# Kernel optimization log

Hardware: AMD Instinct MI355X
Metric: run time of the kernel (lower is better)

## Reference

```python
import jax, jax.numpy as jnp
import numpy as np

NUM_HEADS = 16

def setup_inputs() -> dict:
    key = jax.random.key(0)
    ks = jax.random.split(key, 6)
    S, B, D = 2048, 4, 1280
    return {
        "hidden_states": jax.random.normal(ks[0], (S, B, D), dtype=jnp.float32),
        "rotary_pos_emb": jax.random.normal(ks[1], (S, D // NUM_HEADS // 2), dtype=jnp.float32),
        "in_proj_w": jax.random.normal(ks[2], (3 * D, D), dtype=jnp.float32) * 0.02,
        "in_proj_b": jax.random.normal(ks[3], (3 * D,), dtype=jnp.float32) * 0.02,
        "out_proj_w": jax.random.normal(ks[4], (D, D), dtype=jnp.float32) * 0.02,
        "out_proj_b": jax.random.normal(ks[5], (D,), dtype=jnp.float32) * 0.02,
    }

def _rotate_half(x):
    h = x.shape[-1] // 2
    return jnp.concatenate([-x[..., h:], x[..., :h]], axis=-1)

def _apply_rope(t, cos, sin):
    # t: [B,S,H,Dh]; cos/sin: [1,S,1,Dh]. Compute in fp32 like the original.
    orig = t.dtype
    t32 = t.astype(jnp.float32)
    return (t32 * cos + _rotate_half(t32) * sin).astype(orig)

def reference(hidden_states, rotary_pos_emb, in_proj_w, in_proj_b, out_proj_w, out_proj_b):
    S, B, D = hidden_states.shape
    H = NUM_HEADS
    Dh = D // H

    # Fused QKV projection: [S,B,3D]
    qkv = jnp.einsum('sbd,ed->sbe', hidden_states, in_proj_w) + in_proj_b
    qkv = qkv.reshape(S, B, 3, H, Dh).transpose(2, 1, 0, 3, 4)  # [3,B,S,H,Dh]
    q, k, v = qkv[0], qkv[1], qkv[2]

    # RoPE tables: freqs [S, Dh/2] -> tiled to [1,S,1,Dh] (repeat along last dim)
    cos = jnp.tile(jnp.cos(rotary_pos_emb), (1, 2))[None, :, None, :].astype(jnp.float32)
    sin = jnp.tile(jnp.sin(rotary_pos_emb), (1, 2))[None, :, None, :].astype(jnp.float32)
    q = _apply_rope(q, cos, sin)
    k = _apply_rope(k, cos, sin)

    # [B,H,S,Dh]
    q = q.transpose(0, 2, 1, 3)
    k = k.transpose(0, 2, 1, 3)
    v = v.transpose(0, 2, 1, 3)

    scale = 1.0 / np.sqrt(Dh).astype(np.float32)
    scores = jnp.einsum('bhqd,bhkd->bhqk', q, k) * scale
    attn = jax.nn.softmax(scores, axis=-1)
    out = jnp.einsum('bhqk,bhkd->bhqd', attn, v)  # [B,H,S,Dh]

    out = out.transpose(2, 0, 1, 3).reshape(S, B, D)  # [S,B,D]
    return jnp.einsum('sbd,ed->sbe', out, out_proj_w) + out_proj_b
```

## Files before the change

kernel.cpp:

```cpp
#include <hip/hip_runtime.h>
#include <hip/hip_bf16.h>
#include <math.h>

typedef __bf16 bf16x4 __attribute__((ext_vector_type(4)));
typedef __bf16 bf16x8 __attribute__((ext_vector_type(8)));
typedef float  f32x4  __attribute__((ext_vector_type(4)));

#define S_LEN 2048
#define BATCH 4
#define DMODEL 1280
#define NHEAD 16
#define DHEAD 80
#define KDIM 1280

__device__ __forceinline__ f32x4 mfma_bf16(bf16x8 a, bf16x8 b, f32x4 c) {
  return __builtin_amdgcn_mfma_f32_16x16x32_bf16(a, b, c, 0, 0, 0);
}

__device__ __forceinline__ void gload16(const void* g, void* l) {
  __builtin_amdgcn_global_load_lds(
      (const __attribute__((address_space(1))) unsigned int*)g,
      (__attribute__((address_space(3))) unsigned int*)l, 16, 0, 0);
}

__global__ void cast_f32_to_bf16(const float* __restrict__ in,
                                 __bf16* __restrict__ out, int n4) {
  int i = blockIdx.x * 256 + threadIdx.x;
  if (i >= n4) return;
  float4 v = reinterpret_cast<const float4*>(in)[i];
  bf16x4 o;
  o[0] = (__bf16)v.x; o[1] = (__bf16)v.y; o[2] = (__bf16)v.z; o[3] = (__bf16)v.w;
  reinterpret_cast<bf16x4*>(out)[i] = o;
}

__global__ void build_sincos(const float* __restrict__ rot,
                             float* __restrict__ ctab, float* __restrict__ stab, int n) {
  int i = blockIdx.x * 256 + threadIdx.x;
  if (i >= n) return;
  float v = rot[i];
  ctab[i] = cosf(v);
  stab[i] = sinf(v);
}

__global__ void zero_fill(float* __restrict__ p, int n) {
  int i = blockIdx.x * 256 + threadIdx.x;
  if (i < n) p[i] = 0.0f;
}

__global__ __launch_bounds__(256, 4) void gemm_qkv128(
    const __bf16* __restrict__ A, const __bf16* __restrict__ Bw,
    const float* __restrict__ bias,
    __bf16* __restrict__ qw, __bf16* __restrict__ kw, __bf16* __restrict__ vtw)
{
  __shared__ __align__(1024) char smem[32768];
  const int tid = threadIdx.x;
  const int lane = tid & 63;
  const int w = tid >> 6;
  const int lr = lane & 15, lg = lane >> 4;
  const int wr = w >> 1, wc = w & 1;

  const int wg = blockIdx.x;
  const int xcd = wg & 7, idx = wg >> 3;
  const int bx = xcd * 8 + (idx & 7);
  const int by = idx >> 3;
  const int r0 = bx * 128, c0 = by * 128;
  const char* asrc = (const char*)(A + (size_t)r0 * KDIM);
  const char* bsrc = (const char*)(Bw + (size_t)c0 * KDIM);

  f32x4 acc[4][4] = {};

  for (int t = 0; t < 20; ++t) {
    const size_t kb = (size_t)t * 128;
#pragma unroll
    for (int i = 0; i < 8; ++i) {
      const int L = i * 4096 + tid * 16;
      const int r = (L & 16383) >> 7;
      const int coff = (L & 127) ^ ((r & 7) << 4);
      const char* s = (L < 16384 ? asrc : bsrc) + (size_t)r * 2560 + kb + coff;
      gload16(s, &smem[L]);
    }
    __syncthreads();

#pragma unroll
    for (int kk = 0; kk < 2; ++kk) {
      bf16x8 af[4], bfr[4];
#pragma unroll
      for (int rf = 0; rf < 4; ++rf) {
        const int row = wr * 64 + rf * 16 + lr;
        af[rf] = *reinterpret_cast<const bf16x8*>(
            &smem[row * 128 + ((kk * 64 + lg * 16) ^ ((row & 7) << 4))]);
      }
#pragma unroll
      for (int cf = 0; cf < 4; ++cf) {
        const int row = wc * 64 + cf * 16 + lr;
        bfr[cf] = *reinterpret_cast<const bf16x8*>(
            &smem[16384 + row * 128 + ((kk * 64 + lg * 16) ^ ((row & 7) << 4))]);
      }
#pragma unroll
      for (int rf = 0; rf < 4; ++rf)
#pragma unroll
        for (int cf = 0; cf < 4; ++cf)
          acc[rf][cf] = mfma_bf16(af[rf], bfr[cf], acc[rf][cf]);
    }
    __syncthreads();
  }

  float biasr[4];
#pragma unroll
  for (int cf = 0; cf < 4; ++cf) biasr[cf] = bias[c0 + wc * 64 + cf * 16 + lr];

#pragma unroll
  for (int cf = 0; cf < 4; ++cf) {
    const int col = wc * 64 + cf * 16 + lr;
#pragma unroll
    for (int rf = 0; rf < 4; ++rf)
#pragma unroll
      for (int j = 0; j < 4; ++j) {
        const int row = wr * 64 + rf * 16 + lg * 4 + j;
        *reinterpret_cast<__bf16*>(
            &smem[row * 256 + ((col ^ ((row & 7) << 3)) << 1)]) =
            (__bf16)(acc[rf][cf][j] + biasr[cf]);
      }
  }
  __syncthreads();

  const int which = c0 / DMODEL;
  const int ee0 = c0 - which * DMODEL;

  if (which < 2) {
    __bf16* dst = (which == 0) ? qw : kw;
#pragma unroll
    for (int i = 0; i < 8; ++i) {
      const int cid = i * 256 + tid;
      const int row = cid >> 4, slot = cid & 15;
      bf16x8 v = *reinterpret_cast<const bf16x8*>(
          &smem[row * 256 + ((slot ^ (row & 7)) << 4)]);
      const int tr = r0 + row;
      const int b = tr & 3, stok = tr >> 2;
      const int ee = ee0 + slot * 8;
      const int h = ee / DHEAD, dh = ee - h * DHEAD;
      *reinterpret_cast<bf16x8*>(
          &dst[((size_t)(b * NHEAD + h) * S_LEN + stok) * DHEAD + dh]) = v;
    }
  } else {
    const int s0 = r0 >> 2;
#pragma unroll
    for (int i = 0; i < 8; ++i) {
      const int cid = i * 256 + tid;
      const int col = cid >> 4;
      const int b = (cid >> 2) & 3, spblk = cid & 3;
      bf16x8 v;
#pragma unroll
      for (int k = 0; k < 8; ++k) {
        const int spl = spblk * 8 + k;
        const int sl = (spl & 3) | ((spl & 24) >> 1) | ((spl & 4) << 2);
        const int row = sl * 4 + b;
        v[k] = *reinterpret_cast<const __bf16*>(
            &smem[row * 256 + ((col ^ ((row & 7) << 3)) << 1)]);
      }
      const int ee = ee0 + col;
      const int h = ee / DHEAD, dh = ee - h * DHEAD;
      *reinterpret_cast<bf16x8*>(
          &vtw[((size_t)(b * NHEAD + h) * DHEAD + dh) * S_LEN + s0 + spblk * 8]) = v;
    }
  }
}

template <int MODE>
__global__ __launch_bounds__(256) void gemm_bt(
    const __bf16* __restrict__ A, const __bf16* __restrict__ Bw,
    const float* __restrict__ bias, float* __restrict__ outf)
{
  __shared__ __align__(16) char smem[2][2][16384];
  const int tid = threadIdx.x;
  const int lane = tid & 63;
  const int w = tid >> 6;
  const int lr = lane & 15, lg = lane >> 4;
  const int rowblk = (w >> 1) * 64, colblk = (w & 1) * 64;
  const int sxz = (lane & 7) << 4;

  const int wg = blockIdx.x;
  const int xcd = wg & 7, idx = wg >> 3;
  const int bx = xcd * 8 + (idx & 7);
  const int by = idx >> 3;
  const int r0 = bx * 128;
  const int c0 = by * 128;
  const char* asrc = (const char*)(A + (size_t)r0 * KDIM);
  const char* bsrc = (const char*)(Bw + (size_t)c0 * KDIM);

  f32x4 acc[4][4] = {};

  auto stage = [&](int buf, int kt) {
    const size_t kb = (size_t)kt * 128;
#pragma unroll
    for (int i = 0; i < 4; ++i) {
      int L = i * 4096 + tid * 16;
      int r = L >> 7;
      int coff = (L & 127) ^ ((r & 7) << 4);
      gload16(asrc + (size_t)r * 2560 + kb + coff, &smem[buf][0][L]);
      gload16(bsrc + (size_t)r * 2560 + kb + coff, &smem[buf][1][L]);
    }
  };

  auto compute = [&](int buf) {
#pragma unroll
    for (int kk = 0; kk < 2; ++kk) {
      const int cb = (kk * 64 + lg * 16) ^ sxz;
      bf16x8 af[4], bfr[4];
#pragma unroll
      for (int rf = 0; rf < 4; ++rf)
        af[rf] = *reinterpret_cast<const bf16x8*>(&smem[buf][0][(rowblk + rf * 16 + lr) * 128 + cb]);
#pragma unroll
      for (int cf = 0; cf < 4; ++cf)
        bfr[cf] = *reinterpret_cast<const bf16x8*>(&smem[buf][1][(colblk + cf * 16 + lr) * 128 + cb]);
#pragma unroll
      for (int rf = 0; rf < 4; ++rf)
#pragma unroll
        for (int cf = 0; cf < 4; ++cf)
          acc[rf][cf] = mfma_bf16(af[rf], bfr[cf], acc[rf][cf]);
    }
  };

  stage(0, 0);
  asm volatile("s_waitcnt vmcnt(0)" ::: "memory");
  __builtin_amdgcn_s_barrier();
  __builtin_amdgcn_sched_barrier(0);

  for (int t = 0; t < 20; ++t) {
    const int buf = t & 1;
    if (t < 19) {
      stage(buf ^ 1, t + 1);
      asm volatile("s_waitcnt vmcnt(8)" ::: "memory");
    } else {
      asm volatile("s_waitcnt vmcnt(0)" ::: "memory");
    }
    __builtin_amdgcn_sched_barrier(0);
    __builtin_amdgcn_s_barrier();
    __builtin_amdgcn_sched_barrier(0);

    compute(buf);

    __builtin_amdgcn_sched_barrier(0);
    __builtin_amdgcn_s_barrier();
    __builtin_amdgcn_sched_barrier(0);
  }

  float biasr[4];
#pragma unroll
  for (int cf = 0; cf < 4; ++cf) biasr[cf] = bias[c0 + colblk + cf * 16 + lr];

#pragma unroll
  for (int rf = 0; rf < 4; ++rf)
#pragma unroll
    for (int cf = 0; cf < 4; ++cf) {
      const int c = c0 + colblk + cf * 16 + lr;
#pragma unroll
      for (int j = 0; j < 4; ++j) {
        const int r = r0 + rowblk + rf * 16 + lg * 4 + j;
        outf[(size_t)r * DMODEL + c] = acc[rf][cf][j] + biasr[cf];
      }
    }
}

__global__ void rope_kernel(__bf16* __restrict__ qw, __bf16* __restrict__ kw,
                            const float* __restrict__ ctab, const float* __restrict__ stab,
                            float qscale)
{
  int idx = blockIdx.x * 256 + threadIdx.x;
  const int j = idx % 10;
  int rest = idx / 10;
  const int s = rest & (S_LEN - 1);
  rest >>= 11;
  const int bh = rest & 63;
  const int isk = rest >> 6;
  __bf16* base = (isk ? kw : qw) + ((size_t)bh * S_LEN + s) * DHEAD;
  const float4 c4 = *reinterpret_cast<const float4*>(ctab + s * 40 + j * 4);
  const float4 s4 = *reinterpret_cast<const float4*>(stab + s * 40 + j * 4);
  bf16x4 a = *reinterpret_cast<bf16x4*>(base + j * 4);
  bf16x4 b = *reinterpret_cast<bf16x4*>(base + 40 + j * 4);
  const float m = isk ? 1.0f : qscale;
  const float cc[4] = {c4.x, c4.y, c4.z, c4.w};
  const float ss[4] = {s4.x, s4.y, s4.z, s4.w};
#pragma unroll
  for (int t = 0; t < 4; ++t) {
    float fa = (float)a[t], fb = (float)b[t];
    a[t] = (__bf16)((fa * cc[t] - fb * ss[t]) * m);
    b[t] = (__bf16)((fb * cc[t] + fa * ss[t]) * m);
  }
  *reinterpret_cast<bf16x4*>(base + j * 4) = a;
  *reinterpret_cast<bf16x4*>(base + 40 + j * 4) = b;
}

__global__ __launch_bounds__(256, 2) void attn_kernel(
    const __bf16* __restrict__ qw, const __bf16* __restrict__ kw,
    const __bf16* __restrict__ vtw, __bf16* __restrict__ ow,
    const float* __restrict__ zp)
{
  __shared__ __align__(1024) char smem[2][24576];

  const int tid = threadIdx.x;
  const int lane = tid & 63;
  const int w = tid >> 6;
  const int lr = lane & 15, lg = lane >> 4;

  const int wg = blockIdx.x;
  const int local = wg >> 3;
  const int bh = (wg & 7) * 8 + (local >> 3);
  const int qt = local & 7;

  const char* qbase = (const char*)(qw + ((size_t)bh * S_LEN + qt * 256) * DHEAD);
  const char* kbase = (const char*)(kw + (size_t)bh * S_LEN * DHEAD);
  const char* vbase = (const char*)(vtw + (size_t)bh * DHEAD * S_LEN);
  const char* zpb = (const char*)zp;

  bf16x8 z8, one8;
#pragma unroll
  for (int i = 0; i < 8; ++i) { z8[i] = (__bf16)0.0f; one8[i] = (__bf16)1.0f; }

  bf16x8 aq[4][3];
#pragma unroll
  for (int m = 0; m < 4; ++m) {
    const char* rp = qbase + (size_t)(w * 64 + m * 16 + lr) * 160;
    aq[m][0] = *reinterpret_cast<const bf16x8*>(rp + lg * 16);
    aq[m][1] = *reinterpret_cast<const bf16x8*>(rp + 64 + lg * 16);
    aq[m][2] = (lg < 2) ? *reinterpret_cast<const bf16x8*>(rp + 128 + lg * 16) : z8;
  }

  const char* src[6];
  size_t step[6];
#pragma unroll
  for (int i = 0; i < 6; ++i) {
    const int s = w * 6 + i;
    if (s < 12) {
      const int ks = s >> 2, n = s & 3;
      if (ks == 2 && lg >= 2) { src[i] = zpb + lane * 16; step[i] = 0; }
      else { src[i] = kbase + (size_t)(n * 16 + lr) * 160 + ks * 64 + lg * 16; step[i] = 64 * 160; }
    } else {
      const int v = s - 12, mf = v >> 1, ks2 = v & 1;
      if (mf == 5) { src[i] = zpb + lane * 16; step[i] = 0; }
      else { src[i] = vbase + (size_t)(mf * 16 + lr) * 4096 + (size_t)(ks2 * 32 + lg * 8) * 2; step[i] = 128; }
    }
  }

  auto stage = [&](int buf) {
#pragma unroll
    for (int i = 0; i < 6; ++i) {
      gload16(src[i], &smem[buf][(w * 6 + i) * 1024]);
      src[i] += step[i];
    }
  };

  f32x4 accO[5][4] = {};
  f32x4 accD[4] = {};

  stage(0);
  asm volatile("s_waitcnt vmcnt(0)" ::: "memory");
  __builtin_amdgcn_s_barrier();
  __builtin_amdgcn_sched_barrier(0);

  for (int t = 0; t < 32; ++t) {
    const int buf = t & 1;
    if (t < 31) {
      stage(buf ^ 1);
      asm volatile("s_waitcnt vmcnt(6)" ::: "memory");
    } else {
      asm volatile("s_waitcnt vmcnt(0)" ::: "memory");
    }
    __builtin_amdgcn_sched_barrier(0);
    __builtin_amdgcn_s_barrier();
    __builtin_amdgcn_sched_barrier(0);

    const char* Kb = smem[buf];
    const char* Vb = smem[buf] + 12288;

    f32x4 sc[4][4] = {};
#pragma unroll
    for (int n = 0; n < 4; ++n) {
      bf16x8 af0 = *reinterpret_cast<const bf16x8*>(Kb + (0 * 4 + n) * 1024 + lane * 16);
      bf16x8 af1 = *reinterpret_cast<const bf16x8*>(Kb + (1 * 4 + n) * 1024 + lane * 16);
      bf16x8 af2 = *reinterpret_cast<const bf16x8*>(Kb + (2 * 4 + n) * 1024 + lane * 16);
#pragma unroll
      for (int m = 0; m < 4; ++m) {
        sc[m][n] = mfma_bf16(af0, aq[m][0], sc[m][n]);
        sc[m][n] = mfma_bf16(af1, aq[m][1], sc[m][n]);
        sc[m][n] = mfma_bf16(af2, aq[m][2], sc[m][n]);
      }
    }

    bf16x8 bp[4][2];
#pragma unroll
    for (int m = 0; m < 4; ++m)
#pragma unroll
      for (int n = 0; n < 4; ++n) {
#pragma unroll
        for (int j = 0; j < 4; ++j)
          bp[m][n >> 1][(n & 1) * 4 + j] = (__bf16)__builtin_amdgcn_exp2f(sc[m][n][j]);
      }

#pragma unroll
    for (int ks2 = 0; ks2 < 2; ++ks2) {
#pragma unroll
      for (int mf = 0; mf < 5; ++mf) {
        bf16x8 av = *reinterpret_cast<const bf16x8*>(Vb + (mf * 2 + ks2) * 1024 + lane * 16);
#pragma unroll
        for (int m = 0; m < 4; ++m)
          accO[mf][m] = mfma_bf16(av, bp[m][ks2], accO[mf][m]);
      }
#pragma unroll
      for (int m = 0; m < 4; ++m)
        accD[m] = mfma_bf16(one8, bp[m][ks2], accD[m]);
    }

    __builtin_amdgcn_sched_barrier(0);
    __builtin_amdgcn_s_barrier();
    __builtin_amdgcn_sched_barrier(0);
  }

  __syncthreads();

  float rinv[4];
#pragma unroll
  for (int m = 0; m < 4; ++m) rinv[m] = 1.0f / accD[m][0];

  char* sOut = smem[0];
#pragma unroll
  for (int mf = 0; mf < 5; ++mf)
#pragma unroll
    for (int m = 0; m < 4; ++m) {
      bf16x4 o4;
#pragma unroll
      for (int j = 0; j < 4; ++j) o4[j] = (__bf16)(accO[mf][m][j] * rinv[m]);
      *reinterpret_cast<bf16x4*>(sOut + (size_t)(w * 64 + m * 16 + lr) * 160 + (mf * 16 + lg * 4) * 2) = o4;
    }
  __syncthreads();

  const int b = bh >> 4, h = bh & 15;
#pragma unroll
  for (int i = 0; i < 10; ++i) {
    int c = i * 256 + tid;
    int row = c / 10, slot = c - row * 10;
    int token = (qt * 256 + row) * 4 + b;
    *reinterpret_cast<bf16x8*>((char*)ow + (size_t)token * 2560 + h * 160 + slot * 16) =
        *reinterpret_cast<const bf16x8*>(sOut + row * 160 + slot * 16);
  }
}

extern "C" void kernel_launch(void* const* d_in, const int* in_sizes, int n_in,
                              void* d_out, int out_size, void* d_ws, size_t ws_size,
                              hipStream_t stream)
{
  const float* hidden = (const float*)d_in[0];
  const float* rot    = (const float*)d_in[1];
  const float* w1     = (const float*)d_in[2];
  const float* b1     = (const float*)d_in[3];
  const float* w2     = (const float*)d_in[4];
  const float* b2     = (const float*)d_in[5];
  float* out = (float*)d_out;

  char* ws = (char*)d_ws;
  __bf16* Xbf  = (__bf16*)(ws);
  __bf16* W1bf = (__bf16*)(ws + 20971520);
  __bf16* W2bf = (__bf16*)(ws + 30801920);
  float*  ctab = (float*)(ws + 34078720);
  float*  stab = (float*)(ws + 34406400);
  __bf16* qwp  = (__bf16*)(ws + 34734080);
  __bf16* kwp  = (__bf16*)(ws + 55705600);
  __bf16* vtwp = (__bf16*)(ws + 76677120);
  __bf16* owp  = (__bf16*)(ws + 97648640);
  float*  zp   = (float*)(ws + 118620160);

  cast_f32_to_bf16<<<10240, 256, 0, stream>>>(hidden, Xbf, 2621440);
  cast_f32_to_bf16<<<4800, 256, 0, stream>>>(w1, W1bf, 1228800);
  cast_f32_to_bf16<<<1600, 256, 0, stream>>>(w2, W2bf, 409600);
  build_sincos<<<320, 256, 0, stream>>>(rot, ctab, stab, 81920);
  zero_fill<<<4, 256, 0, stream>>>(zp, 1024);

  gemm_qkv128<<<1920, 256, 0, stream>>>(Xbf, W1bf, b1, qwp, kwp, vtwp);

  const float qscale = 1.4426950408889634f / sqrtf(80.0f);
  rope_kernel<<<10240, 256, 0, stream>>>(qwp, kwp, ctab, stab, qscale);

  attn_kernel<<<512, 256, 0, stream>>>(qwp, kwp, vtwp, owp, zp);

  gemm_bt<1><<<640, 256, 0, stream>>>(owp, W2bf, b2, out);
}
```

Baseline: 247.6 us.

## Single-buffer output GEMM for higher occupancy and add MFMA priority hints in attention

The output projection GEMM drops double buffering in favour of a single 32KB LDS tile with plain __syncthreads, and sets launch_bounds to 4 blocks per CU. The aim is to hide memory latency through more resident workgroups rather than software prefetch. The attention kernel separately wraps its two MFMA phases in s_setprio so waves issuing matrix work get priority over waves doing exp2. The GEMM change gives up in-block load/compute overlap, and the priority hints may or may not change scheduling.

```diff
diff --git a/kernel.cpp b/kernel.cpp
--- a/kernel.cpp
+++ b/kernel.cpp
@@ -166,97 +166,75 @@
   }
 }
 
-template <int MODE>
-__global__ __launch_bounds__(256) void gemm_bt(
+__global__ __launch_bounds__(256, 4) void gemm_out128(
     const __bf16* __restrict__ A, const __bf16* __restrict__ Bw,
     const float* __restrict__ bias, float* __restrict__ outf)
 {
-  __shared__ __align__(16) char smem[2][2][16384];
+  __shared__ __align__(1024) char smem[32768];
   const int tid = threadIdx.x;
   const int lane = tid & 63;
   const int w = tid >> 6;
   const int lr = lane & 15, lg = lane >> 4;
-  const int rowblk = (w >> 1) * 64, colblk = (w & 1) * 64;
-  const int sxz = (lane & 7) << 4;
+  const int wr = w >> 1, wc = w & 1;
 
   const int wg = blockIdx.x;
   const int xcd = wg & 7, idx = wg >> 3;
   const int bx = xcd * 8 + (idx & 7);
   const int by = idx >> 3;
-  const int r0 = bx * 128;
-  const int c0 = by * 128;
+  const int r0 = bx * 128, c0 = by * 128;
   const char* asrc = (const char*)(A + (size_t)r0 * KDIM);
   const char* bsrc = (const char*)(Bw + (size_t)c0 * KDIM);
 
   f32x4 acc[4][4] = {};
 
-  auto stage = [&](int buf, int kt) {
-    const size_t kb = (size_t)kt * 128;
-#pragma unroll
-    for (int i = 0; i < 4; ++i) {
-      int L = i * 4096 + tid * 16;
-      int r = L >> 7;
-      int coff = (L & 127) ^ ((r & 7) << 4);
-      gload16(asrc + (size_t)r * 2560 + kb + coff, &smem[buf][0][L]);
-      gload16(bsrc + (size_t)r * 2560 + kb + coff, &smem[buf][1][L]);
-    }
-  };
-
-  auto compute = [&](int buf) {
+  for (int t = 0; t < 20; ++t) {
+    const size_t kb = (size_t)t * 128;
+#pragma unroll
+    for (int i = 0; i < 8; ++i) {
+      const int L = i * 4096 + tid * 16;
+      const int r = (L & 16383) >> 7;
+      const int coff = (L & 127) ^ ((r & 7) << 4);
+      const char* s = (L < 16384 ? asrc : bsrc) + (size_t)r * 2560 + kb + coff;
+      gload16(s, &smem[L]);
+    }
+    __syncthreads();
+
 #pragma unroll
     for (int kk = 0; kk < 2; ++kk) {
-      const int cb = (kk * 64 + lg * 16) ^ sxz;
       bf16x8 af[4], bfr[4];
 #pragma unroll
-      for (int rf = 0; rf < 4; ++rf)
-        af[rf] = *reinterpret_cast<const bf16x8*>(&smem[buf][0][(rowblk + rf * 16 + lr) * 128 + cb]);
-#pragma unroll
-      for (int cf = 0; cf < 4; ++cf)
-        bfr[cf] = *reinterpret_cast<const bf16x8*>(&smem[buf][1][(colblk + cf * 16 + lr) * 128 + cb]);
+      for (int rf = 0; rf < 4; ++rf) {
+        const int row = wr * 64 + rf * 16 + lr;
+        af[rf] = *reinterpret_cast<const bf16x8*>(
+            &smem[row * 128 + ((kk * 64 + lg * 16) ^ ((row & 7) << 4))]);
+      }
+#pragma unroll
+      for (int cf = 0; cf < 4; ++cf) {
+        const int row = wc * 64 + cf * 16 + lr;
+        bfr[cf] = *reinterpret_cast<const bf16x8*>(
+            &smem[16384 + row * 128 + ((kk * 64 + lg * 16) ^ ((row & 7) << 4))]);
+      }
 #pragma unroll
       for (int rf = 0; rf < 4; ++rf)
 #pragma unroll
         for (int cf = 0; cf < 4; ++cf)
           acc[rf][cf] = mfma_bf16(af[rf], bfr[cf], acc[rf][cf]);
     }
-  };
-
-  stage(0, 0);
-  asm volatile("s_waitcnt vmcnt(0)" ::: "memory");
-  __builtin_amdgcn_s_barrier();
-  __builtin_amdgcn_sched_barrier(0);
-
-  for (int t = 0; t < 20; ++t) {
-    const int buf = t & 1;
-    if (t < 19) {
-      stage(buf ^ 1, t + 1);
-      asm volatile("s_waitcnt vmcnt(8)" ::: "memory");
-    } else {
-      asm volatile("s_waitcnt vmcnt(0)" ::: "memory");
-    }
-    __builtin_amdgcn_sched_barrier(0);
-    __builtin_amdgcn_s_barrier();
-    __builtin_amdgcn_sched_barrier(0);
-
-    compute(buf);
-
-    __builtin_amdgcn_sched_barrier(0);
-    __builtin_amdgcn_s_barrier();
-    __builtin_amdgcn_sched_barrier(0);
+    __syncthreads();
   }
 
   float biasr[4];
 #pragma unroll
-  for (int cf = 0; cf < 4; ++cf) biasr[cf] = bias[c0 + colblk + cf * 16 + lr];
+  for (int cf = 0; cf < 4; ++cf) biasr[cf] = bias[c0 + wc * 64 + cf * 16 + lr];
 
 #pragma unroll
   for (int rf = 0; rf < 4; ++rf)
 #pragma unroll
     for (int cf = 0; cf < 4; ++cf) {
-      const int c = c0 + colblk + cf * 16 + lr;
+      const int c = c0 + wc * 64 + cf * 16 + lr;
 #pragma unroll
       for (int j = 0; j < 4; ++j) {
-        const int r = r0 + rowblk + rf * 16 + lg * 4 + j;
+        const int r = r0 + wr * 64 + rf * 16 + lg * 4 + j;
         outf[(size_t)r * DMODEL + c] = acc[rf][cf][j] + biasr[cf];
       }
     }
@@ -374,6 +352,7 @@
     const char* Vb = smem[buf] + 12288;
 
     f32x4 sc[4][4] = {};
+    __builtin_amdgcn_s_setprio(1);
 #pragma unroll
     for (int n = 0; n < 4; ++n) {
       bf16x8 af0 = *reinterpret_cast<const bf16x8*>(Kb + (0 * 4 + n) * 1024 + lane * 16);
@@ -386,6 +365,7 @@
         sc[m][n] = mfma_bf16(af2, aq[m][2], sc[m][n]);
       }
     }
+    __builtin_amdgcn_s_setprio(0);
 
     bf16x8 bp[4][2];
 #pragma unroll
@@ -397,6 +377,7 @@
           bp[m][n >> 1][(n & 1) * 4 + j] = (__bf16)__builtin_amdgcn_exp2f(sc[m][n][j]);
       }
 
+    __builtin_amdgcn_s_setprio(1);
 #pragma unroll
     for (int ks2 = 0; ks2 < 2; ++ks2) {
 #pragma unroll
@@ -410,6 +391,7 @@
       for (int m = 0; m < 4; ++m)
         accD[m] = mfma_bf16(one8, bp[m][ks2], accD[m]);
     }
+    __builtin_amdgcn_s_setprio(0);
 
     __builtin_amdgcn_sched_barrier(0);
     __builtin_amdgcn_s_barrier();
@@ -482,5 +464,5 @@
 
   attn_kernel<<<512, 256, 0, stream>>>(qwp, kwp, vtwp, owp, zp);
 
-  gemm_bt<1><<<640, 256, 0, stream>>>(owp, W2bf, b2, out);
-}
+  gemm_out128<<<640, 256, 0, stream>>>(owp, W2bf, b2, out);
+}
```

Result: faster. 234.7 us (-5.2%).
